# Performance work log

Hardware: AMD Instinct MI355X
Metric: run time of the kernel (lower is better)

## Reference

```python
import jax, jax.numpy as jnp
import numpy as np

B, N, F_IN, F_OUT, E = 8, 2048, 512, 256, 5
ALPHA = 0.2  # leaky relu slope
NEG = -9e15


def setup_inputs() -> dict:
    key = jax.random.key(0)
    ks = jax.random.split(key, 11)
    s_in = 1.0 / np.sqrt(F_IN)
    s_out = 1.0 / np.sqrt(F_OUT)
    s_e = 1.0 / np.sqrt(E)
    return {
        "feat": jax.random.normal(ks[0], (B, N, F_IN), jnp.float32),
        "adj": jax.random.randint(ks[1], (B, N, N), 0, 2, jnp.int32),
        "W": jax.random.normal(ks[2], (F_IN, F_OUT), jnp.float32) * s_in,
        "W_1": jax.random.normal(ks[3], (F_IN, F_OUT), jnp.float32) * s_in,
        "W_2": jax.random.normal(ks[4], (F_IN, F_OUT), jnp.float32) * s_in,
        "a_1": jax.random.normal(ks[5], (F_OUT, 1), jnp.float32) * s_out,
        "a_2": jax.random.normal(ks[6], (F_OUT, 1), jnp.float32) * s_out,
        "a_12": jax.random.normal(ks[7], (F_OUT, F_OUT), jnp.float32) * s_out,
        "L_w": jax.random.normal(ks[8], (E, F_IN), jnp.float32) * s_in,
        "R_w": jax.random.normal(ks[9], (E, F_IN), jnp.float32) * s_in,
        "B_w": jax.random.normal(ks[10], (F_OUT, E, E), jnp.float32) * s_e,
    }


def reference(feat, adj, W, W_1, W_2, a_1, a_2, a_12, L_w, R_w, B_w):
    # --- attention ---
    h = jnp.einsum('bnf,fd->bnd', feat, W)                 # [B,N,D]
    Ax = jnp.einsum('bnd,do->bno', h, a_1)[..., 0]         # [B,N] (score of target)
    Ay = jnp.einsum('bnd,do->bno', h, a_2)[..., 0]         # [B,N] (score of source)
    A_xy = jnp.einsum('bid,de,bje->bij', h, a_12, h)       # [B,N,N] bilinear term
    logits = Ax[:, None, :] + Ay[:, :, None] + A_xy        # [B,N,N]
    e = jnp.where(logits > 0, logits, ALPHA * logits)      # leaky relu
    e = jnp.where(adj > 0, e, NEG)
    attention = jax.nn.softmax(e, axis=-1)                 # dropout p=0 / eval -> identity
    # --- aggregate ---
    feat_agg = jnp.einsum('bij,bjf->bif', attention, feat) # [B,N,F_IN]
    # --- update ---
    h_1 = jnp.einsum('bnf,fd->bnd', feat, W_1)
    h_2 = jnp.einsum('bnf,fd->bnd', feat_agg, W_2)
    e1 = jnp.einsum('bnf,ef->bne', feat, L_w)              # [B,N,E]
    e2 = jnp.einsum('bnf,ef->bne', feat_agg, R_w)          # [B,N,E]
    h_12 = jnp.einsum('bni,oij,bnj->bno', e1, B_w, e2)     # [B,N,F_OUT]
    return h_1 + h_2 + h_12  # activation=None -> identity
```

## Files before the change

kernel.cpp:

```cpp
#include <hip/hip_runtime.h>
#include <hip/hip_bf16.h>

#define BB 8
#define NN 2048
#define FIN 512
#define FOUT 256
#define EE 5
#define ALPHA_ 0.2f
#define NEGV -9e15f
#define JW 512

typedef __hip_bfloat16 bf16;
typedef __bf16 bf16x8 __attribute__((ext_vector_type(8)));
typedef float f32x4 __attribute__((ext_vector_type(4)));
typedef unsigned long long u64;

__device__ __forceinline__ float bf2f(bf16 x) { return __bfloat162float(x); }
__device__ __forceinline__ bf16 f2bf(float x) { return __float2bfloat16(x); }

__device__ __forceinline__ void async16(const bf16* g, bf16* l) {
    __builtin_amdgcn_global_load_lds(
        (const __attribute__((address_space(1))) void*)g,
        (__attribute__((address_space(3))) void*)l, 16, 0, 0);
}


__global__ void split_f32_bf16(const float* __restrict__ in,
                               bf16* __restrict__ hi, bf16* __restrict__ lo) {
    long i = ((long)blockIdx.x * blockDim.x + threadIdx.x) * 8;
    float4 a = *(const float4*)(&in[i]);
    float4 b = *(const float4*)(&in[i + 4]);
    float x[8] = { a.x, a.y, a.z, a.w, b.x, b.y, b.z, b.w };
    bf16 th[8], tl[8];
    for (int k = 0; k < 8; k++) {
        th[k] = f2bf(x[k]);
        tl[k] = f2bf(x[k] - bf2f(th[k]));
    }
    *(uint4*)(&hi[i]) = *(const uint4*)th;
    *(uint4*)(&lo[i]) = *(const uint4*)tl;
}

__global__ void pack_adj(const int* __restrict__ adj, u64* __restrict__ adjm) {
    long wid = (((long)blockIdx.x * 256) + threadIdx.x) >> 6;
    int lane = threadIdx.x & 63;
    long base = wid * 256;
    for (int c = 0; c < 4; c++) {
        int a = adj[base + c * 64 + lane];
        u64 m = __ballot(a > 0);
        if (lane == 0) adjm[base / 64 + c] = m;
    }
}

__global__ void transpose_split(const float* __restrict__ in,
                                bf16* __restrict__ hi, bf16* __restrict__ lo,
                                int R, int C) {
    __shared__ bf16 th[32][33], tl[32][33];
    int c0 = blockIdx.x * 32, r0 = blockIdx.y * 32;
    int x = threadIdx.x, y = threadIdx.y;
    for (int k = 0; k < 4; k++) {
        int r = y + k * 8;
        float f = in[(long)(r0 + r) * C + c0 + x];
        bf16 h = f2bf(f);
        th[r][x] = h;
        tl[r][x] = f2bf(f - bf2f(h));
    }
    __syncthreads();
    for (int k = 0; k < 4; k++) {
        int r = y + k * 8;
        hi[(long)(c0 + r) * R + r0 + x] = th[x][r];
        lo[(long)(c0 + r) * R + r0 + x] = tl[x][r];
    }
}

__global__ void transpose_f32_bf16(const float* __restrict__ in, bf16* __restrict__ out,
                                   int R, int C, long sin_b, long sout_b) {
    __shared__ bf16 tile[32][33];
    long bi = (long)blockIdx.z * sin_b;
    long bo = (long)blockIdx.z * sout_b;
    int c0 = blockIdx.x * 32, r0 = blockIdx.y * 32;
    int x = threadIdx.x, y = threadIdx.y;
    for (int k = 0; k < 4; k++) {
        int r = y + k * 8;
        tile[r][x] = f2bf(in[bi + (long)(r0 + r) * C + c0 + x]);
    }
    __syncthreads();
    for (int k = 0; k < 4; k++) {
        int r = y + k * 8;
        out[bo + (long)(c0 + r) * R + r0 + x] = tile[x][r];
    }
}

__global__ __launch_bounds__(256) void gemm_bt_split(
        const bf16* __restrict__ Ah, const bf16* __restrict__ Al,
        const bf16* __restrict__ Bh, const bf16* __restrict__ Bl,
        bf16* __restrict__ Chi, bf16* __restrict__ Clo,
        const float* __restrict__ bias, int Nn, int K) {
    __shared__ alignas(16) bf16 Ash[128 * 32], Asl[128 * 32];
    __shared__ alignas(16) bf16 Bsh[128 * 32], Bsl[128 * 32];
    int tid = threadIdx.x;
    int lane = tid & 63, ww = tid >> 6;
    int wm = ww >> 1, wn = ww & 1;
    int quad = lane >> 4, l16 = lane & 15;
    int qx = quad ^ ((l16 >> 1) & 3);
    int sseg = (tid & 3) ^ ((tid >> 3) & 3);
    int m0 = blockIdx.x * 128, n0 = blockIdx.y * 128;
    f32x4 acc[4][4] = {};
    for (int k0 = 0; k0 < K; k0 += 32) {
#pragma unroll
        for (int i = 0; i < 2; i++) {
            int idx = tid + i * 256;
            int row = idx >> 2;
            long ao = (long)(m0 + row) * K + k0 + sseg * 8;
            long bo = (long)(n0 + row) * K + k0 + sseg * 8;
            async16(&Ah[ao], &Ash[idx * 8]);
            async16(&Al[ao], &Asl[idx * 8]);
            async16(&Bh[bo], &Bsh[idx * 8]);
            async16(&Bl[bo], &Bsl[idx * 8]);
        }
        __syncthreads();
        bf16x8 afh[4], afl[4], bfh[4], bfl[4];
        for (int mi = 0; mi < 4; mi++) {
            int so = (wm * 64 + mi * 16 + l16) * 32 + qx * 8;
            afh[mi] = *(const bf16x8*)(&Ash[so]);
            afl[mi] = *(const bf16x8*)(&Asl[so]);
        }
        for (int ni = 0; ni < 4; ni++) {
            int so = (wn * 64 + ni * 16 + l16) * 32 + qx * 8;
            bfh[ni] = *(const bf16x8*)(&Bsh[so]);
            bfl[ni] = *(const bf16x8*)(&Bsl[so]);
        }
        for (int mi = 0; mi < 4; mi++)
            for (int ni = 0; ni < 4; ni++) {
                acc[mi][ni] = __builtin_amdgcn_mfma_f32_16x16x32_bf16(afh[mi], bfh[ni], acc[mi][ni], 0, 0, 0);
                acc[mi][ni] = __builtin_amdgcn_mfma_f32_16x16x32_bf16(afh[mi], bfl[ni], acc[mi][ni], 0, 0, 0);
                acc[mi][ni] = __builtin_amdgcn_mfma_f32_16x16x32_bf16(afl[mi], bfh[ni], acc[mi][ni], 0, 0, 0);
            }
        __syncthreads();
    }
    for (int mi = 0; mi < 4; mi++)
        for (int ni = 0; ni < 4; ni++) {
            int col = n0 + wn * 64 + ni * 16 + l16;
            float bv = bias ? bias[col] : 0.f;
            for (int r = 0; r < 4; r++) {
                int row = m0 + wm * 64 + mi * 16 + quad * 4 + r;
                float v = acc[mi][ni][r] + bv;
                bf16 h = f2bf(v);
                Chi[(long)row * Nn + col] = h;
                Clo[(long)row * Nn + col] = f2bf(v - bf2f(h));
            }
        }
}

__global__ __launch_bounds__(256) void gemm_bt(
        const bf16* __restrict__ A, const bf16* __restrict__ Bt,
        bf16* __restrict__ C, int Nn, int K, long sA, long sB, long sC) {
    __shared__ alignas(16) bf16 As[128 * 32];
    __shared__ alignas(16) bf16 Bs[128 * 32];
    const bf16* Ab = A + (long)blockIdx.z * sA;
    const bf16* Bb = Bt + (long)blockIdx.z * sB;
    bf16* Cb = C + (long)blockIdx.z * sC;
    int tid = threadIdx.x;
    int lane = tid & 63, ww = tid >> 6;
    int wm = ww >> 1, wn = ww & 1;
    int quad = lane >> 4, l16 = lane & 15;
    int qx = quad ^ ((l16 >> 1) & 3);
    int sseg = (tid & 3) ^ ((tid >> 3) & 3);
    int m0 = blockIdx.x * 128, n0 = blockIdx.y * 128;
    f32x4 acc[4][4] = {};
    for (int k0 = 0; k0 < K; k0 += 32) {
#pragma unroll
        for (int i = 0; i < 2; i++) {
            int idx = tid + i * 256;
            int row = idx >> 2;
            async16(&Ab[(long)(m0 + row) * K + k0 + sseg * 8], &As[idx * 8]);
            async16(&Bb[(long)(n0 + row) * K + k0 + sseg * 8], &Bs[idx * 8]);
        }
        __syncthreads();
        bf16x8 af[4], bfr[4];
        for (int mi = 0; mi < 4; mi++)
            af[mi] = *(const bf16x8*)(&As[(wm * 64 + mi * 16 + l16) * 32 + qx * 8]);
        for (int ni = 0; ni < 4; ni++)
            bfr[ni] = *(const bf16x8*)(&Bs[(wn * 64 + ni * 16 + l16) * 32 + qx * 8]);
        for (int mi = 0; mi < 4; mi++)
            for (int ni = 0; ni < 4; ni++)
                acc[mi][ni] = __builtin_amdgcn_mfma_f32_16x16x32_bf16(
                    af[mi], bfr[ni], acc[mi][ni], 0, 0, 0);
        __syncthreads();
    }
    for (int mi = 0; mi < 4; mi++)
        for (int ni = 0; ni < 4; ni++) {
            int col = n0 + wn * 64 + ni * 16 + l16;
            for (int r = 0; r < 4; r++) {
                int row = m0 + wm * 64 + mi * 16 + quad * 4 + r;
                Cb[(long)row * Nn + col] = f2bf(acc[mi][ni][r]);
            }
        }
}

__global__ void ay_kernel(const bf16* __restrict__ hh, const bf16* __restrict__ hl,
                          const float* __restrict__ a2, float* __restrict__ Ay) {
    int lane = threadIdx.x & 63, w = threadIdx.x >> 6;
    long row = (long)blockIdx.x * 4 + w;
    float p = 0.f;
    for (int i = 0; i < 4; i++) {
        int d = i * 64 + lane;
        p += (bf2f(hh[row * FOUT + d]) + bf2f(hl[row * FOUT + d])) * a2[d];
    }
    for (int off = 32; off; off >>= 1) p += __shfl_xor(p, off);
    if (lane == 0) Ay[row] = p;
}

__global__ __launch_bounds__(256) void pass_score(
        const bf16* __restrict__ qh_, const bf16* __restrict__ ql_,
        const bf16* __restrict__ hh_, const bf16* __restrict__ hl_,
        const u64* __restrict__ adjm, const float* __restrict__ Ay,
        float* __restrict__ mpm, float* __restrict__ mpl,
        bf16* __restrict__ P) {
    __shared__ alignas(16) bf16 Hsh[2][128 * 32], Hsl[2][128 * 32];
    __shared__ alignas(16) bf16 pst[4][16 * 64];
    int tid = threadIdx.x;
    int lane = tid & 63, w = tid >> 6;
    int quad = lane >> 4, l16 = lane & 15;
    int qx = quad ^ ((l16 >> 1) & 3);
    int sseg = (tid & 3) ^ ((tid >> 3) & 3);
    int b = blockIdx.z, jz = blockIdx.y;
    int i0 = blockIdx.x * 64 + w * 16;
    long qoff = ((long)b * NN + i0) * FOUT;
    const bf16* hbh = hh_ + ((long)b * NN + (long)jz * JW) * FOUT;
    const bf16* hbl = hl_ + ((long)b * NN + (long)jz * JW) * FOUT;
    const u64* amb = adjm + ((long)b * NN + i0) * (NN / 64) + jz * (JW / 64);
    bf16* pw = pst[w];

    bf16x8 qfh[8], qfl[8];
#pragma unroll
    for (int kk = 0; kk < 8; kk++) {
        qfh[kk] = *(const bf16x8*)(&qh_[qoff + (long)l16 * FOUT + kk * 32 + quad * 8]);
        qfl[kk] = *(const bf16x8*)(&ql_[qoff + (long)l16 * FOUT + kk * 32 + quad * 8]);
    }
    float ay_[4];
#pragma unroll
    for (int r = 0; r < 4; r++) ay_[r] = Ay[(long)b * NN + i0 + quad * 4 + r];

    float m_[4], l_[4];
#pragma unroll
    for (int r = 0; r < 4; r++) { m_[r] = -3.0e38f; l_[r] = 0.f; }

    auto STAGE = [&](int jc, int kk, int buf) {
#pragma unroll
        for (int i = 0; i < 2; i++) {
            int idx = tid + i * 256;
            int row = idx >> 2;
            long go = (long)(jc * 128 + row) * FOUT + kk * 32 + sseg * 8;
            async16(&hbh[go], &Hsh[buf][idx * 8]);
            async16(&hbl[go], &Hsl[buf][idx * 8]);
        }
    };

    f32x4 sacc[8];
#pragma unroll
    for (int ni = 0; ni < 8; ni++) sacc[ni] = (f32x4){0.f, 0.f, 0.f, 0.f};

    STAGE(0, 0, 0);
    for (int jc = 0; jc < 4; jc++) {
#pragma unroll
        for (int kk = 0; kk < 8; kk++) {
            const int cur = kk & 1;
            if (kk < 7)           STAGE(jc, kk + 1, cur ^ 1);
            else if (jc < 3)      STAGE(jc + 1, 0, cur ^ 1);
            if (kk == 0) {
                if (jc == 0) asm volatile("s_waitcnt vmcnt(4)" ::: "memory");
                else         asm volatile("s_waitcnt vmcnt(8)" ::: "memory");
            } else if (kk == 7 && jc == 3) {
                asm volatile("s_waitcnt vmcnt(0)" ::: "memory");
            } else {
                asm volatile("s_waitcnt vmcnt(4)" ::: "memory");
            }
            __builtin_amdgcn_s_barrier();
            __builtin_amdgcn_sched_barrier(0);

            __builtin_amdgcn_s_setprio(1);
#pragma unroll
            for (int ni = 0; ni < 8; ni++) {
                int so = (ni * 16 + l16) * 32 + qx * 8;
                bf16x8 hfh = *(const bf16x8*)(&Hsh[cur][so]);
                bf16x8 hfl = *(const bf16x8*)(&Hsl[cur][so]);
                sacc[ni] = __builtin_amdgcn_mfma_f32_16x16x32_bf16(qfh[kk], hfh, sacc[ni], 0, 0, 0);
                sacc[ni] = __builtin_amdgcn_mfma_f32_16x16x32_bf16(qfh[kk], hfl, sacc[ni], 0, 0, 0);
                sacc[ni] = __builtin_amdgcn_mfma_f32_16x16x32_bf16(qfl[kk], hfh, sacc[ni], 0, 0, 0);
            }
            __builtin_amdgcn_s_setprio(0);

            if (kk == 7) {
                u64 am[4][2];
#pragma unroll
                for (int r = 0; r < 4; r++) {
                    am[r][0] = amb[(long)(quad * 4 + r) * (NN / 64) + jc * 2 + 0];
                    am[r][1] = amb[(long)(quad * 4 + r) * (NN / 64) + jc * 2 + 1];
                }
#pragma unroll
                for (int ni = 0; ni < 8; ni++)
#pragma unroll
                    for (int r = 0; r < 4; r++) {
                        float v = sacc[ni][r] + ay_[r];
                        v = v > 0.f ? v : ALPHA_ * v;
                        int bit = (int)((am[r][ni >> 2] >> ((ni * 16 + l16) & 63)) & 1);
                        sacc[ni][r] = bit ? v : NEGV;
                    }
#pragma unroll
                for (int r = 0; r < 4; r++) {
                    float mc = -3.0e38f;
#pragma unroll
                    for (int ni = 0; ni < 8; ni++) mc = fmaxf(mc, sacc[ni][r]);
                    for (int off = 8; off; off >>= 1) mc = fmaxf(mc, __shfl_xor(mc, off));
                    float mnew = fmaxf(m_[r], mc);
                    float scale = __expf(m_[r] - mnew);
                    float ps = 0.f;
#pragma unroll
                    for (int ni = 0; ni < 8; ni++) {
                        float p = __expf(sacc[ni][r] - mnew);
                        sacc[ni][r] = p;
                        ps += p;
                    }
                    for (int off = 8; off; off >>= 1) ps += __shfl_xor(ps, off);
                    l_[r] = l_[r] * scale + ps;
                    m_[r] = mnew;
                    if (l16 == 0)
                        mpm[(((long)b * 4 + jz) * 4 + jc) * NN + i0 + quad * 4 + r] = mnew;
                }
#pragma unroll
                for (int h = 0; h < 2; h++) {
#pragma unroll
                    for (int ni = 0; ni < 4; ni++)
#pragma unroll
                        for (int r = 0; r < 4; r++) {
                            int row = quad * 4 + r;
                            int byt = (row * 128 + (ni * 16 + l16) * 2) ^ ((row & 7) << 4);
                            *(bf16*)((char*)pw + byt) = f2bf(sacc[h * 4 + ni][r]);
                        }
#pragma unroll
                    for (int s2 = 0; s2 < 2; s2++) {
                        int cq = quad + s2 * 4;
                        int byt = (l16 * 128 + cq * 16) ^ ((l16 & 7) << 4);
                        uint4 v = *(const uint4*)((const char*)pw + byt);
                        *(uint4*)(&P[((long)b * NN + i0 + l16) * NN + (long)jz * JW
                                     + jc * 128 + h * 64 + cq * 8]) = v;
                    }
                }
#pragma unroll
                for (int ni = 0; ni < 8; ni++) sacc[ni] = (f32x4){0.f, 0.f, 0.f, 0.f};
            }
            __builtin_amdgcn_sched_barrier(0);
            __builtin_amdgcn_s_barrier();
            __builtin_amdgcn_sched_barrier(0);
        }
    }
    if (l16 == 0)
#pragma unroll
        for (int r = 0; r < 4; r++)
            mpl[((long)b * 4 + jz) * NN + i0 + quad * 4 + r] = l_[r];
}

__global__ void ml_merge(const float* __restrict__ mpm, const float* __restrict__ mpl,
                         float2* __restrict__ mlfin) {
    long row = (long)blockIdx.x * blockDim.x + threadIdx.x;
    long b = row / NN, n = row % NN;
    float mw[4];
    float m = -3.0e38f;
    for (int jz = 0; jz < 4; jz++) {
        mw[jz] = mpm[((b * 4 + jz) * 4 + 3) * NN + n];
        m = fmaxf(m, mw[jz]);
    }
    float l = 0.f;
    for (int jz = 0; jz < 4; jz++)
        l += mpl[(b * 4 + jz) * NN + n] * __expf(mw[jz] - m);
    mlfin[row] = make_float2(m, 1.f / l);
}

__global__ __launch_bounds__(256) void fixup_p(
        bf16* __restrict__ P, const float* __restrict__ mpm,
        const float2* __restrict__ mlfin) {
    int row = blockIdx.x, b = blockIdx.y;
    int t = threadIdx.x;
    int jz = t >> 6, jc = (t >> 4) & 3;
    float2 mf = mlfin[(long)b * NN + row];
    float scale = __expf(mpm[(((long)b * 4 + jz) * 4 + jc) * NN + row] - mf.x) * mf.y;
    long base = ((long)b * NN + row) * NN + t * 8;
    uint4 v = *(const uint4*)(&P[base]);
    bf16* pv = (bf16*)&v;
    bf16 o[8];
    for (int k = 0; k < 8; k++) o[k] = f2bf(bf2f(pv[k]) * scale);
    *(uint4*)(&P[base]) = *(const uint4*)o;
}

__global__ void e_kernel(const bf16* __restrict__ X, const float* __restrict__ Wt,
                         float* __restrict__ out) {
    int lane = threadIdx.x & 63, w = threadIdx.x >> 6;
    long row = (long)blockIdx.x * 4 + w;
    uint4 raw = *(const uint4*)(&X[row * FIN + lane * 8]);
    const bf16* xp = (const bf16*)&raw;
    float xv[8];
    for (int i = 0; i < 8; i++) xv[i] = bf2f(xp[i]);
    for (int e = 0; e < EE; e++) {
        float4 w0 = *(const float4*)(&Wt[e * FIN + lane * 8]);
        float4 w1 = *(const float4*)(&Wt[e * FIN + lane * 8 + 4]);
        float p = xv[0] * w0.x + xv[1] * w0.y + xv[2] * w0.z + xv[3] * w0.w
                + xv[4] * w1.x + xv[5] * w1.y + xv[6] * w1.z + xv[7] * w1.w;
        for (int off = 32; off; off >>= 1) p += __shfl_xor(p, off);
        if (lane == 0) out[row * EE + e] = p;
    }
}

__global__ void final_kernel(float* __restrict__ out,
                             const bf16* __restrict__ h1, const bf16* __restrict__ h2,
                             const float* __restrict__ e1, const float* __restrict__ e2,
                             const float* __restrict__ Bw) {
    long row = blockIdx.x;
    int o = threadIdx.x;
    float a[EE], c[EE];
    for (int i = 0; i < EE; i++) { a[i] = e1[row * EE + i]; c[i] = e2[row * EE + i]; }
    const float* bw = Bw + (long)o * EE * EE;
    float acc = 0.f;
    for (int i = 0; i < EE; i++)
        for (int j = 0; j < EE; j++)
            acc += bw[i * EE + j] * a[i] * c[j];
    long idx = row * FOUT + o;
    out[idx] = acc + bf2f(h1[idx]) + bf2f(h2[idx]);
}

extern "C" void kernel_launch(void* const* d_in, const int* in_sizes, int n_in,
                              void* d_out, int out_size, void* d_ws, size_t ws_size,
                              hipStream_t stream) {
    const float* feat = (const float*)d_in[0];
    const int*   adj  = (const int*)d_in[1];
    const float* W    = (const float*)d_in[2];
    const float* W1   = (const float*)d_in[3];
    const float* W2   = (const float*)d_in[4];
    const float* a1   = (const float*)d_in[5];
    const float* a2   = (const float*)d_in[6];
    const float* a12  = (const float*)d_in[7];
    const float* Lw   = (const float*)d_in[8];
    const float* Rw   = (const float*)d_in[9];
    const float* Bw   = (const float*)d_in[10];
    float* out = (float*)d_out;

    char* ws = (char*)d_ws;
    size_t off = 0;
    auto alloc = [&](size_t bytes) {
        char* p = ws + off;
        off += (bytes + 255) & ~(size_t)255;
        return p;
    };
    bf16* WTh  = (bf16*)alloc((size_t)FOUT * FIN * 2);
    bf16* WTl  = (bf16*)alloc((size_t)FOUT * FIN * 2);
    bf16* W1T  = (bf16*)alloc((size_t)FOUT * FIN * 2);
    bf16* W2T  = (bf16*)alloc((size_t)FOUT * FIN * 2);
    bf16* aTh  = (bf16*)alloc((size_t)FOUT * FOUT * 2);
    bf16* aTl  = (bf16*)alloc((size_t)FOUT * FOUT * 2);
    bf16* fh   = (bf16*)alloc((size_t)BB * NN * FIN * 2);
    bf16* fl   = (bf16*)alloc((size_t)BB * NN * FIN * 2);
    bf16* hh   = (bf16*)alloc((size_t)BB * NN * FOUT * 2);
    bf16* hl   = (bf16*)alloc((size_t)BB * NN * FOUT * 2);
    bf16* featT= (bf16*)alloc((size_t)BB * NN * FIN * 2);
    float* Ay  = (float*)alloc((size_t)BB * NN * 4);
    float* mpm = (float*)alloc((size_t)BB * 4 * 4 * NN * 4);
    float* mpl = (float*)alloc((size_t)BB * 4 * NN * 4);
    float2* mlfin = (float2*)alloc((size_t)BB * NN * 8);
    float* e1  = (float*)alloc((size_t)BB * NN * EE * 4);
    float* e2  = (float*)alloc((size_t)BB * NN * EE * 4);
    u64* adjm  = (u64*)alloc((size_t)BB * NN * (NN / 64) * 8);
    bf16* P    = (bf16*)alloc((size_t)BB * NN * NN * 2);
    bf16* qh   = (bf16*)d_out;
    bf16* ql   = qh + (size_t)BB * NN * FOUT;
    bf16* fagg = fl;
    bf16* h1   = hh;
    bf16* h2   = hl;

    dim3 tb(32, 8, 1);
    split_f32_bf16<<<(BB * NN * FIN) / (256 * 8), 256, 0, stream>>>(feat, fh, fl);
    pack_adj<<<(BB * NN * NN) / (256 * 4), 256, 0, stream>>>(adj, adjm);
    transpose_split<<<dim3(FOUT / 32, FIN / 32, 1), tb, 0, stream>>>(W, WTh, WTl, FIN, FOUT);
    transpose_split<<<dim3(FOUT / 32, FOUT / 32, 1), tb, 0, stream>>>(a12, aTh, aTl, FOUT, FOUT);
    transpose_f32_bf16<<<dim3(FOUT / 32, FIN / 32, 1), tb, 0, stream>>>(W1, W1T, FIN, FOUT, 0, 0);
    transpose_f32_bf16<<<dim3(FOUT / 32, FIN / 32, 1), tb, 0, stream>>>(W2, W2T, FIN, FOUT, 0, 0);
    transpose_f32_bf16<<<dim3(FIN / 32, NN / 32, BB), tb, 0, stream>>>(
        feat, featT, NN, FIN, (long)NN * FIN, (long)FIN * NN);
    gemm_bt_split<<<dim3(BB * NN / 128, FOUT / 128, 1), 256, 0, stream>>>(
        fh, fl, WTh, WTl, hh, hl, nullptr, FOUT, FIN);
    ay_kernel<<<BB * NN / 4, 256, 0, stream>>>(hh, hl, a2, Ay);
    gemm_bt_split<<<dim3(BB * NN / 128, FOUT / 128, 1), 256, 0, stream>>>(
        hh, hl, aTh, aTl, qh, ql, a1, FOUT, FOUT);
    pass_score<<<dim3(NN / 64, 4, BB), 256, 0, stream>>>(
        qh, ql, hh, hl, adjm, Ay, mpm, mpl, P);
    ml_merge<<<(BB * NN) / 256, 256, 0, stream>>>(mpm, mpl, mlfin);
    fixup_p<<<dim3(NN, BB, 1), 256, 0, stream>>>(P, mpm, mlfin);
    gemm_bt<<<dim3(NN / 128, FIN / 128, BB), 256, 0, stream>>>(
        P, featT, fagg, FIN, NN, (long)NN * NN, (long)FIN * NN, (long)NN * FIN);
    gemm_bt<<<dim3(BB * NN / 128, FOUT / 128, 1), 256, 0, stream>>>(
        fh, W1T, h1, FOUT, FIN, 0, 0, 0);
    gemm_bt<<<dim3(BB * NN / 128, FOUT / 128, 1), 256, 0, stream>>>(
        fagg, W2T, h2, FOUT, FIN, 0, 0, 0);
    e_kernel<<<BB * NN / 4, 256, 0, stream>>>(fh, Lw, e1);
    e_kernel<<<BB * NN / 4, 256, 0, stream>>>(fagg, Rw, e2);
    final_kernel<<<BB * NN, FOUT, 0, stream>>>(out, h1, h2, e1, e2, Bw);
}
```

Before: 544.8 us.

## Fold softmax rescaling into PV GEMM and double rows per wave in score pass

Removes the fixup_p kernel, which rescaled the whole BxNxN bf16 P matrix in place. The PV GEMM now applies per-chunk running-max correction factors to its accumulators at each 128-column boundary and multiplies by a final normalisation factor at the epilogue. This saves a full read and write of P (64 MB). Separately, pass_score now handles 32 rows per wave (two 16-row M tiles), so each staged H tile feeds twice as many MFMAs. It uses launch_bounds(256,2) and adjusts the vmcnt wait count, at the cost of higher register pressure and half as many blocks.

```diff
diff --git a/kernel.cpp b/kernel.cpp
--- a/kernel.cpp
+++ b/kernel.cpp
@@ -197,6 +197,72 @@
         }
 }
 
+__global__ __launch_bounds__(256) void gemm_pv(
+        const bf16* __restrict__ A, const bf16* __restrict__ Bt,
+        bf16* __restrict__ C, const float* __restrict__ rs,
+        const float* __restrict__ fin) {
+    __shared__ alignas(16) bf16 As[128 * 32];
+    __shared__ alignas(16) bf16 Bs[128 * 32];
+    int b = blockIdx.z;
+    const bf16* Ab = A + (long)b * NN * NN;
+    const bf16* Bb = Bt + (long)b * FIN * NN;
+    bf16* Cb = C + (long)b * NN * FIN;
+    int tid = threadIdx.x;
+    int lane = tid & 63, ww = tid >> 6;
+    int wm = ww >> 1, wn = ww & 1;
+    int quad = lane >> 4, l16 = lane & 15;
+    int qx = quad ^ ((l16 >> 1) & 3);
+    int sseg = (tid & 3) ^ ((tid >> 3) & 3);
+    int m0 = blockIdx.x * 128, n0 = blockIdx.y * 128;
+    f32x4 acc[4][4] = {};
+    for (int k0 = 0; k0 < NN; k0 += 32) {
+        if (k0 && !(k0 & 127)) {
+            int c = k0 >> 7;
+#pragma unroll
+            for (int mi = 0; mi < 4; mi++) {
+                float4 rv = *(const float4*)(&rs[((long)b * 16 + c) * NN
+                                                 + m0 + wm * 64 + mi * 16 + quad * 4]);
+#pragma unroll
+                for (int ni = 0; ni < 4; ni++) {
+                    acc[mi][ni][0] *= rv.x;
+                    acc[mi][ni][1] *= rv.y;
+                    acc[mi][ni][2] *= rv.z;
+                    acc[mi][ni][3] *= rv.w;
+                }
+            }
+        }
+#pragma unroll
+        for (int i = 0; i < 2; i++) {
+            int idx = tid + i * 256;
+            int row = idx >> 2;
+            async16(&Ab[(long)(m0 + row) * NN + k0 + sseg * 8], &As[idx * 8]);
+            async16(&Bb[(long)(n0 + row) * NN + k0 + sseg * 8], &Bs[idx * 8]);
+        }
+        __syncthreads();
+        bf16x8 af[4], bfr[4];
+        for (int mi = 0; mi < 4; mi++)
+            af[mi] = *(const bf16x8*)(&As[(wm * 64 + mi * 16 + l16) * 32 + qx * 8]);
+        for (int ni = 0; ni < 4; ni++)
+            bfr[ni] = *(const bf16x8*)(&Bs[(wn * 64 + ni * 16 + l16) * 32 + qx * 8]);
+        for (int mi = 0; mi < 4; mi++)
+            for (int ni = 0; ni < 4; ni++)
+                acc[mi][ni] = __builtin_amdgcn_mfma_f32_16x16x32_bf16(
+                    af[mi], bfr[ni], acc[mi][ni], 0, 0, 0);
+        __syncthreads();
+    }
+    for (int mi = 0; mi < 4; mi++) {
+        float4 fv = *(const float4*)(&fin[(long)b * NN + m0 + wm * 64 + mi * 16 + quad * 4]);
+        for (int ni = 0; ni < 4; ni++) {
+            int col = n0 + wn * 64 + ni * 16 + l16;
+            float fvr[4] = { fv.x, fv.y, fv.z, fv.w };
+            for (int r = 0; r < 4; r++) {
+                int row = m0 + wm * 64 + mi * 16 + quad * 4 + r;
+                Cb[(long)row * FIN + col] = f2bf(acc[mi][ni][r] * fvr[r]);
+            }
+        }
+    }
+}
+
 __global__ void ay_kernel(const bf16* __restrict__ hh, const bf16* __restrict__ hl,
                           const float* __restrict__ a2, float* __restrict__ Ay) {
     int lane = threadIdx.x & 63, w = threadIdx.x >> 6;
@@ -210,7 +276,7 @@
     if (lane == 0) Ay[row] = p;
 }
 
-__global__ __launch_bounds__(256) void pass_score(
+__global__ __launch_bounds__(256, 2) void pass_score(
         const bf16* __restrict__ qh_, const bf16* __restrict__ ql_,
         const bf16* __restrict__ hh_, const bf16* __restrict__ hl_,
         const u64* __restrict__ adjm, const float* __restrict__ Ay,
@@ -224,26 +290,34 @@
     int qx = quad ^ ((l16 >> 1) & 3);
     int sseg = (tid & 3) ^ ((tid >> 3) & 3);
     int b = blockIdx.z, jz = blockIdx.y;
-    int i0 = blockIdx.x * 64 + w * 16;
-    long qoff = ((long)b * NN + i0) * FOUT;
+    int iw = blockIdx.x * 128 + w * 32;
     const bf16* hbh = hh_ + ((long)b * NN + (long)jz * JW) * FOUT;
     const bf16* hbl = hl_ + ((long)b * NN + (long)jz * JW) * FOUT;
-    const u64* amb = adjm + ((long)b * NN + i0) * (NN / 64) + jz * (JW / 64);
+    const u64* amb = adjm + ((long)b * NN + iw) * (NN / 64) + jz * (JW / 64);
     bf16* pw = pst[w];
 
-    bf16x8 qfh[8], qfl[8];
-#pragma unroll
-    for (int kk = 0; kk < 8; kk++) {
-        qfh[kk] = *(const bf16x8*)(&qh_[qoff + (long)l16 * FOUT + kk * 32 + quad * 8]);
-        qfl[kk] = *(const bf16x8*)(&ql_[qoff + (long)l16 * FOUT + kk * 32 + quad * 8]);
-    }
-    float ay_[4];
-#pragma unroll
-    for (int r = 0; r < 4; r++) ay_[r] = Ay[(long)b * NN + i0 + quad * 4 + r];
-
-    float m_[4], l_[4];
-#pragma unroll
-    for (int r = 0; r < 4; r++) { m_[r] = -3.0e38f; l_[r] = 0.f; }
+    bf16x8 qfh[2][8], qfl[2][8];
+#pragma unroll
+    for (int mi = 0; mi < 2; mi++) {
+        long qoff = ((long)b * NN + iw + mi * 16 + l16) * FOUT;
+#pragma unroll
+        for (int kk = 0; kk < 8; kk++) {
+            qfh[mi][kk] = *(const bf16x8*)(&qh_[qoff + kk * 32 + quad * 8]);
+            qfl[mi][kk] = *(const bf16x8*)(&ql_[qoff + kk * 32 + quad * 8]);
+        }
+    }
+    float ay_[2][4];
+#pragma unroll
+    for (int mi = 0; mi < 2; mi++)
+#pragma unroll
+        for (int r = 0; r < 4; r++)
+            ay_[mi][r] = Ay[(long)b * NN + iw + mi * 16 + quad * 4 + r];
+
+    float m_[2][4], l_[2][4];
+#pragma unroll
+    for (int mi = 0; mi < 2; mi++)
+#pragma unroll
+        for (int r = 0; r < 4; r++) { m_[mi][r] = -3.0e38f; l_[mi][r] = 0.f; }
 
     auto STAGE = [&](int jc, int kk, int buf) {
 #pragma unroll
@@ -256,9 +330,11 @@
         }
     };
 
-    f32x4 sacc[8];
-#pragma unroll
-    for (int ni = 0; ni < 8; ni++) sacc[ni] = (f32x4){0.f, 0.f, 0.f, 0.f};
+    f32x4 sacc[2][8];
+#pragma unroll
+    for (int mi = 0; mi < 2; mi++)
+#pragma unroll
+        for (int ni = 0; ni < 8; ni++) sacc[mi][ni] = (f32x4){0.f, 0.f, 0.f, 0.f};
 
     STAGE(0, 0, 0);
     for (int jc = 0; jc < 4; jc++) {
@@ -269,7 +345,7 @@
             else if (jc < 3)      STAGE(jc + 1, 0, cur ^ 1);
             if (kk == 0) {
                 if (jc == 0) asm volatile("s_waitcnt vmcnt(4)" ::: "memory");
-                else         asm volatile("s_waitcnt vmcnt(8)" ::: "memory");
+                else         asm volatile("s_waitcnt vmcnt(20)" ::: "memory");
             } else if (kk == 7 && jc == 3) {
                 asm volatile("s_waitcnt vmcnt(0)" ::: "memory");
             } else {
@@ -284,70 +360,77 @@
                 int so = (ni * 16 + l16) * 32 + qx * 8;
                 bf16x8 hfh = *(const bf16x8*)(&Hsh[cur][so]);
                 bf16x8 hfl = *(const bf16x8*)(&Hsl[cur][so]);
-                sacc[ni] = __builtin_amdgcn_mfma_f32_16x16x32_bf16(qfh[kk], hfh, sacc[ni], 0, 0, 0);
-                sacc[ni] = __builtin_amdgcn_mfma_f32_16x16x32_bf16(qfh[kk], hfl, sacc[ni], 0, 0, 0);
-                sacc[ni] = __builtin_amdgcn_mfma_f32_16x16x32_bf16(qfl[kk], hfh, sacc[ni], 0, 0, 0);
+#pragma unroll
+                for (int mi = 0; mi < 2; mi++) {
+                    sacc[mi][ni] = __builtin_amdgcn_mfma_f32_16x16x32_bf16(qfh[mi][kk], hfh, sacc[mi][ni], 0, 0, 0);
+                    sacc[mi][ni] = __builtin_amdgcn_mfma_f32_16x16x32_bf16(qfh[mi][kk], hfl, sacc[mi][ni], 0, 0, 0);
+                    sacc[mi][ni] = __builtin_amdgcn_mfma_f32_16x16x32_bf16(qfl[mi][kk], hfh, sacc[mi][ni], 0, 0, 0);
+                }
             }
             __builtin_amdgcn_s_setprio(0);
 
             if (kk == 7) {
-                u64 am[4][2];
-#pragma unroll
-                for (int r = 0; r < 4; r++) {
-                    am[r][0] = amb[(long)(quad * 4 + r) * (NN / 64) + jc * 2 + 0];
-                    am[r][1] = amb[(long)(quad * 4 + r) * (NN / 64) + jc * 2 + 1];
+#pragma unroll
+                for (int mi = 0; mi < 2; mi++) {
+                    u64 am[4][2];
+#pragma unroll
+                    for (int r = 0; r < 4; r++) {
+                        long ro = (long)(mi * 16 + quad * 4 + r) * (NN / 64) + jc * 2;
+                        am[r][0] = amb[ro + 0];
+                        am[r][1] = amb[ro + 1];
+                    }
+#pragma unroll
+                    for (int ni = 0; ni < 8; ni++)
+#pragma unroll
+                        for (int r = 0; r < 4; r++) {
+                            float v = sacc[mi][ni][r] + ay_[mi][r];
+                            v = v > 0.f ? v : ALPHA_ * v;
+                            int bit = (int)((am[r][ni >> 2] >> ((ni * 16 + l16) & 63)) & 1);
+                            sacc[mi][ni][r] = bit ? v : NEGV;
+                        }
+#pragma unroll
+                    for (int r = 0; r < 4; r++) {
+                        float mc = -3.0e38f;
+#pragma unroll
+                        for (int ni = 0; ni < 8; ni++) mc = fmaxf(mc, sacc[mi][ni][r]);
+                        for (int off = 8; off; off >>= 1) mc = fmaxf(mc, __shfl_xor(mc, off));
+                        float mnew = fmaxf(m_[mi][r], mc);
+                        float scale = __expf(m_[mi][r] - mnew);
+                        float ps = 0.f;
+#pragma unroll
+                        for (int ni = 0; ni < 8; ni++) {
+                            float p = __expf(sacc[mi][ni][r] - mnew);
+                            sacc[mi][ni][r] = p;
+                            ps += p;
+                        }
+                        for (int off = 8; off; off >>= 1) ps += __shfl_xor(ps, off);
+                        l_[mi][r] = l_[mi][r] * scale + ps;
+                        m_[mi][r] = mnew;
+                        if (l16 == 0)
+                            mpm[(((long)b * 4 + jz) * 4 + jc) * NN + iw + mi * 16 + quad * 4 + r] = mnew;
+                    }
+#pragma unroll
+                    for (int h = 0; h < 2; h++) {
+#pragma unroll
+                        for (int ni = 0; ni < 4; ni++)
+#pragma unroll
+                            for (int r = 0; r < 4; r++) {
+                                int row = quad * 4 + r;
+                                int byt = (row * 128 + (ni * 16 + l16) * 2) ^ ((row & 7) << 4);
+                                *(bf16*)((char*)pw + byt) = f2bf(sacc[mi][h * 4 + ni][r]);
+                            }
+#pragma unroll
+                        for (int s2 = 0; s2 < 2; s2++) {
+                            int cq = quad + s2 * 4;
+                            int byt = (l16 * 128 + cq * 16) ^ ((l16 & 7) << 4);
+                            uint4 v = *(const uint4*)((const char*)pw + byt);
+                            *(uint4*)(&P[((long)b * NN + iw + mi * 16 + l16) * NN + (long)jz * JW
+                                         + jc * 128 + h * 64 + cq * 8]) = v;
+                        }
+                    }
+#pragma unroll
+                    for (int ni = 0; ni < 8; ni++) sacc[mi][ni] = (f32x4){0.f, 0.f, 0.f, 0.f};
                 }
-#pragma unroll
-                for (int ni = 0; ni < 8; ni++)
-#pragma unroll
-                    for (int r = 0; r < 4; r++) {
-                        float v = sacc[ni][r] + ay_[r];
-                        v = v > 0.f ? v : ALPHA_ * v;
-                        int bit = (int)((am[r][ni >> 2] >> ((ni * 16 + l16) & 63)) & 1);
-                        sacc[ni][r] = bit ? v : NEGV;
-                    }
-#pragma unroll
-                for (int r = 0; r < 4; r++) {
-                    float mc = -3.0e38f;
-#pragma unroll
-                    for (int ni = 0; ni < 8; ni++) mc = fmaxf(mc, sacc[ni][r]);
-                    for (int off = 8; off; off >>= 1) mc = fmaxf(mc, __shfl_xor(mc, off));
-                    float mnew = fmaxf(m_[r], mc);
-                    float scale = __expf(m_[r] - mnew);
-                    float ps = 0.f;
-#pragma unroll
-                    for (int ni = 0; ni < 8; ni++) {
-                        float p = __expf(sacc[ni][r] - mnew);
-                        sacc[ni][r] = p;
-                        ps += p;
-                    }
-                    for (int off = 8; off; off >>= 1) ps += __shfl_xor(ps, off);
-                    l_[r] = l_[r] * scale + ps;
-                    m_[r] = mnew;
-                    if (l16 == 0)
-                        mpm[(((long)b * 4 + jz) * 4 + jc) * NN + i0 + quad * 4 + r] = mnew;
-                }
-#pragma unroll
-                for (int h = 0; h < 2; h++) {
-#pragma unroll
-                    for (int ni = 0; ni < 4; ni++)
-#pragma unroll
-                        for (int r = 0; r < 4; r++) {
-                            int row = quad * 4 + r;
-                            int byt = (row * 128 + (ni * 16 + l16) * 2) ^ ((row & 7) << 4);
-                            *(bf16*)((char*)pw + byt) = f2bf(sacc[h * 4 + ni][r]);
-                        }
-#pragma unroll
-                    for (int s2 = 0; s2 < 2; s2++) {
-                        int cq = quad + s2 * 4;
-                        int byt = (l16 * 128 + cq * 16) ^ ((l16 & 7) << 4);
-                        uint4 v = *(const uint4*)((const char*)pw + byt);
-                        *(uint4*)(&P[((long)b * NN + i0 + l16) * NN + (long)jz * JW
-                                     + jc * 128 + h * 64 + cq * 8]) = v;
-                    }
-                }
-#pragma unroll
-                for (int ni = 0; ni < 8; ni++) sacc[ni] = (f32x4){0.f, 0.f, 0.f, 0.f};
             }
             __builtin_amdgcn_sched_barrier(0);
             __builtin_amdgcn_s_barrier();
@@ -356,40 +439,28 @@
     }
     if (l16 == 0)
 #pragma unroll
-        for (int r = 0; r < 4; r++)
-            mpl[((long)b * 4 + jz) * NN + i0 + quad * 4 + r] = l_[r];
+        for (int mi = 0; mi < 2; mi++)
+#pragma unroll
+            for (int r = 0; r < 4; r++)
+                mpl[((long)b * 4 + jz) * NN + iw + mi * 16 + quad * 4 + r] = l_[mi][r];
 }
 
 __global__ void ml_merge(const float* __restrict__ mpm, const float* __restrict__ mpl,
-                         float2* __restrict__ mlfin) {
+                         float* __restrict__ rs, float* __restrict__ fin) {
     long row = (long)blockIdx.x * blockDim.x + threadIdx.x;
     long b = row / NN, n = row % NN;
-    float mw[4];
-    float m = -3.0e38f;
-    for (int jz = 0; jz < 4; jz++) {
-        mw[jz] = mpm[((b * 4 + jz) * 4 + 3) * NN + n];
-        m = fmaxf(m, mw[jz]);
-    }
+    float mc[16];
+#pragma unroll
+    for (int c = 0; c < 16; c++) mc[c] = mpm[(b * 16 + c) * NN + n];
+    float m = fmaxf(fmaxf(mc[3], mc[7]), fmaxf(mc[11], mc[15]));
     float l = 0.f;
+#pragma unroll
     for (int jz = 0; jz < 4; jz++)
-        l += mpl[(b * 4 + jz) * NN + n] * __expf(mw[jz] - m);
-    mlfin[row] = make_float2(m, 1.f / l);
-}
-
-__global__ __launch_bounds__(256) void fixup_p(
-        bf16* __restrict__ P, const float* __restrict__ mpm,
-        const float2* __restrict__ mlfin) {
-    int row = blockIdx.x, b = blockIdx.y;
-    int t = threadIdx.x;
-    int jz = t >> 6, jc = (t >> 4) & 3;
-    float2 mf = mlfin[(long)b * NN + row];
-    float scale = __expf(mpm[(((long)b * 4 + jz) * 4 + jc) * NN + row] - mf.x) * mf.y;
-    long base = ((long)b * NN + row) * NN + t * 8;
-    uint4 v = *(const uint4*)(&P[base]);
-    bf16* pv = (bf16*)&v;
-    bf16 o[8];
-    for (int k = 0; k < 8; k++) o[k] = f2bf(bf2f(pv[k]) * scale);
-    *(uint4*)(&P[base]) = *(const uint4*)o;
+        l += mpl[(b * 4 + jz) * NN + n] * __expf(mc[jz * 4 + 3] - m);
+    fin[row] = __expf(mc[15] - m) / l;
+#pragma unroll
+    for (int c = 1; c < 16; c++)
+        rs[(b * 16 + c) * NN + n] = __expf(mc[c - 1] - mc[c]);
 }
 
 __global__ void e_kernel(const bf16* __restrict__ X, const float* __restrict__ Wt,
@@ -464,7 +535,8 @@
     float* Ay  = (float*)alloc((size_t)BB * NN * 4);
     float* mpm = (float*)alloc((size_t)BB * 4 * 4 * NN * 4);
     float* mpl = (float*)alloc((size_t)BB * 4 * NN * 4);
-    float2* mlfin = (float2*)alloc((size_t)BB * NN * 8);
+    float* rs  = (float*)alloc((size_t)BB * 16 * NN * 4);
+    float* fin = (float*)alloc((size_t)BB * NN * 4);
     float* e1  = (float*)alloc((size_t)BB * NN * EE * 4);
     float* e2  = (float*)alloc((size_t)BB * NN * EE * 4);
     u64* adjm  = (u64*)alloc((size_t)BB * NN * (NN / 64) * 8);
@@ -489,12 +561,11 @@
     ay_kernel<<<BB * NN / 4, 256, 0, stream>>>(hh, hl, a2, Ay);
     gemm_bt_split<<<dim3(BB * NN / 128, FOUT / 128, 1), 256, 0, stream>>>(
         hh, hl, aTh, aTl, qh, ql, a1, FOUT, FOUT);
-    pass_score<<<dim3(NN / 64, 4, BB), 256, 0, stream>>>(
+    pass_score<<<dim3(NN / 128, 4, BB), 256, 0, stream>>>(
         qh, ql, hh, hl, adjm, Ay, mpm, mpl, P);
-    ml_merge<<<(BB * NN) / 256, 256, 0, stream>>>(mpm, mpl, mlfin);
-    fixup_p<<<dim3(NN, BB, 1), 256, 0, stream>>>(P, mpm, mlfin);
-    gemm_bt<<<dim3(NN / 128, FIN / 128, BB), 256, 0, stream>>>(
-        P, featT, fagg, FIN, NN, (long)NN * NN, (long)FIN * NN, (long)NN * FIN);
+    ml_merge<<<(BB * NN) / 256, 256, 0, stream>>>(mpm, mpl, rs, fin);
+    gemm_pv<<<dim3(NN / 128, FIN / 128, BB), 256, 0, stream>>>(
+        P, featT, fagg, rs, fin);
     gemm_bt<<<dim3(BB * NN / 128, FOUT / 128, 1), 256, 0, stream>>>(
         fh, W1T, h1, FOUT, FIN, 0, 0, 0);
     gemm_bt<<<dim3(BB * NN / 128, FOUT / 128, 1), 256, 0, stream>>>(
```

After: 549.4 us. Within noise of the previous version (+0.8%).
